# Kernel tuning notes

Measured on AMD Instinct MI355X. Metric: run time of the kernel, lower is better.

Reference implementation:

```python
import jax, jax.numpy as jnp
import numpy as np

HIDDEN = 2048
QUANTILES = 16
BATCH = 8192
HALF = HIDDEN // 2


def setup_inputs() -> dict:
    key = jax.random.key(0)
    kx, k1, kb1, k2 = jax.random.split(key, 4)
    x = jax.random.normal(kx, (BATCH, HIDDEN), dtype=jnp.float32)
    # Stacked per-head params: head q computes Linear(H->H/2) -> GELU -> Linear(H/2->1)
    # PyTorch Linear default init ~ U(-1/sqrt(fan_in), 1/sqrt(fan_in)); last layer kaiming-normal, bias 0.
    lim1 = 1.0 / np.sqrt(HIDDEN)
    W1 = jax.random.uniform(k1, (QUANTILES, HIDDEN, HALF), minval=-lim1, maxval=lim1, dtype=jnp.float32)
    b1 = jax.random.uniform(kb1, (QUANTILES, HALF), minval=-lim1, maxval=lim1, dtype=jnp.float32)
    # kaiming_normal fan_in, linear nonlinearity -> std = 1/sqrt(fan_in)
    W2 = jax.random.normal(k2, (QUANTILES, HALF), dtype=jnp.float32) / np.sqrt(HALF)
    b2 = jnp.zeros((QUANTILES,), dtype=jnp.float32)
    return {"x": x, "W1": W1, "b1": b1, "W2": W2, "b2": b2}


def reference(x, W1, b1, W2, b2):
    # Batched over all quantile heads: one grouped GEMM + fused GELU + grouped GEMV.
    # h: [batch, quantiles, half]
    h = jnp.einsum('bh,qhk->bqk', x, W1) + b1[None, :, :]
    h = jax.nn.gelu(h, approximate=False)  # torch nn.GELU() default = exact erf GELU
    # out: [batch, quantiles]
    out = jnp.einsum('bqk,qk->bq', h, W2) + b2[None, :]
    return out
```

## Files before the change

### kernel.cpp

```cpp
#include <hip/hip_runtime.h>

#define HIDDEN 2048
#define QUANT  16
#define BATCH  8192
#define HALFD  1024

#define BM 256
#define BN 256
#define BKT 32
#define NT (HIDDEN / BKT)
#define A_HALFS (BM * BKT)
#define SLOT_HALFS (2 * A_HALFS)

typedef _Float16 half8  __attribute__((ext_vector_type(8)));
typedef float    floatx16 __attribute__((ext_vector_type(16)));

__device__ __forceinline__ void load_lds16(const void* gptr, void* lptr) {
  __builtin_amdgcn_global_load_lds(
      (const __attribute__((address_space(1))) void*)gptr,
      (__attribute__((address_space(3))) void*)lptr, 16, 0, 0);
}

__device__ __forceinline__ float gelu_exact(float v) {
  const float z  = 0.7071067811865476f * v;
  const float az = fabsf(z);
  const float t  = __builtin_amdgcn_rcpf(1.0f + 0.3275911f * az);
  const float p  = t * (0.254829592f +
                   t * (-0.284496736f +
                   t * (1.421413741f +
                   t * (-1.453152027f +
                   t * 1.061405429f))));
  float er = 1.0f - p * __expf(-az * az);
  er = copysignf(er, z);
  return 0.5f * v * (1.0f + er);
}

__global__ __launch_bounds__(256) void convert_x_kernel(const float* __restrict__ x,
                                                        _Float16* __restrict__ xh) {
  const int i = (blockIdx.x * 256 + threadIdx.x) * 8;
  const float4 a = *(const float4*)(x + i);
  const float4 b = *(const float4*)(x + i + 4);
  half8 h;
  h[0] = (_Float16)a.x; h[1] = (_Float16)a.y; h[2] = (_Float16)a.z; h[3] = (_Float16)a.w;
  h[4] = (_Float16)b.x; h[5] = (_Float16)b.y; h[6] = (_Float16)b.z; h[7] = (_Float16)b.w;
  *(half8*)(xh + i) = h;
}

__global__ __launch_bounds__(256) void transpose_w1_kernel(const float* __restrict__ W1,
                                                           _Float16* __restrict__ W1T) {
  __shared__ float tile[64][33];
  const int q  = blockIdx.z;
  const int h0 = blockIdx.y * 64;
  const int n0 = blockIdx.x * 32;
  const float* src = W1 + (size_t)q * HIDDEN * HALFD;
  _Float16*    dst = W1T + (size_t)q * HALFD * HIDDEN;
  const int t  = threadIdx.x;
  const int lr = t >> 3;
  const int lc = (t & 7) * 4;
  #pragma unroll
  for (int j = 0; j < 2; ++j) {
    const float4 v = *(const float4*)(src + (size_t)(h0 + lr + 32 * j) * HALFD + n0 + lc);
    tile[lr + 32 * j][lc + 0] = v.x;
    tile[lr + 32 * j][lc + 1] = v.y;
    tile[lr + 32 * j][lc + 2] = v.z;
    tile[lr + 32 * j][lc + 3] = v.w;
  }
  __syncthreads();
  const int sn = t >> 3;
  const int sh = (t & 7) * 8;
  half8 v;
  #pragma unroll
  for (int c = 0; c < 8; ++c) v[c] = (_Float16)tile[sh + c][sn];
  *(half8*)(dst + (size_t)(n0 + sn) * HIDDEN + h0 + sh) = v;
}

__global__ __launch_bounds__(256) void init_out_kernel(float* __restrict__ out,
                                                       const float* __restrict__ b2) {
  const int i = blockIdx.x * 256 + threadIdx.x;
  out[i] = b2[i & (QUANT - 1)];
}

__global__ __launch_bounds__(512, 2) void qhead_gemm_kernel(
    const _Float16* __restrict__ A,
    const _Float16* __restrict__ BT,
    const float* __restrict__ b1,
    const float* __restrict__ W2,
    float* __restrict__ out) {
  extern __shared__ _Float16 lds[];

  const int tid  = threadIdx.x;
  const int lane = tid & 63;
  const int wave = tid >> 6;
  const int wm = wave >> 2, wn = wave & 3;
  const int r31 = lane & 31, l5 = lane >> 5;
  const int fsw = (r31 >> 1) & 3;

  const int flat = blockIdx.x;
  const int wg = (flat & 7) * 256 + (flat >> 3);
  const int mb = wg >> 6;
  const int qn = wg & 63;
  const int q  = qn >> 2;
  const int nb = qn & 3;
  const int m0 = mb << 8;

  const _Float16* Ablk = A + (size_t)m0 * HIDDEN;
  const _Float16* Bblk = BT + ((size_t)q * HALFD + nb * BN) * HIDDEN;

  const int srow = tid >> 2;
  const int skg  = (tid & 3) ^ ((srow >> 1) & 3);
  const _Float16* agp = Ablk + (size_t)srow * HIDDEN + skg * 8;
  const _Float16* bgp = Bblk + (size_t)srow * HIDDEN + skg * 8;

  int aoff[4], boff[2];
  #pragma unroll
  for (int mf = 0; mf < 4; ++mf) aoff[mf] = (wm * 128 + mf * 32 + r31) * BKT;
  #pragma unroll
  for (int nf = 0; nf < 2; ++nf) boff[nf] = (wn * 64 + nf * 32 + r31) * BKT + A_HALFS;

  floatx16 acc[4][2];
  #pragma unroll
  for (int mf = 0; mf < 4; ++mf)
    #pragma unroll
    for (int nf = 0; nf < 2; ++nf)
      #pragma unroll
      for (int i = 0; i < 16; ++i) acc[mf][nf][i] = 0.f;

#define STAGE(ts_) do {                                                    \
    const int ts = (ts_);                                                  \
    const int kc = ((ts < NT) ? ts : (ts - NT)) * BKT;   \
    _Float16* ld = lds + (ts & 3) * SLOT_HALFS + tid * 8;                  \
    load_lds16(agp + kc, ld);                                              \
    load_lds16(agp + kc + (size_t)128 * HIDDEN, ld + 4096);                \
    load_lds16(bgp + kc, ld + A_HALFS);                                    \
    load_lds16(bgp + kc + (size_t)128 * HIDDEN, ld + A_HALFS + 4096);      \
  } while (0)

  STAGE(0); STAGE(1); STAGE(2);
  asm volatile("s_waitcnt vmcnt(8)\n\ts_barrier" ::: "memory");

  #pragma unroll 4
  for (int t = 0; t < NT; ++t) {
    STAGE(t + 3);
    const _Float16* ls = lds + (t & 3) * SLOT_HALFS;
    __builtin_amdgcn_s_setprio(1);
    #pragma unroll
    for (int ks = 0; ks < 2; ++ks) {
      const int p = (((ks << 1) | l5) ^ fsw) << 3;
      half8 af[4], bf[2];
      #pragma unroll
      for (int mf = 0; mf < 4; ++mf) af[mf] = *(const half8*)(ls + aoff[mf] + p);
      #pragma unroll
      for (int nf = 0; nf < 2; ++nf) bf[nf] = *(const half8*)(ls + boff[nf] + p);
      #pragma unroll
      for (int mf = 0; mf < 4; ++mf)
        #pragma unroll
        for (int nf = 0; nf < 2; ++nf)
          acc[mf][nf] = __builtin_amdgcn_mfma_f32_32x32x16_f16(af[mf], bf[nf], acc[mf][nf], 0, 0, 0);
    }
    __builtin_amdgcn_s_setprio(0);
    asm volatile("s_waitcnt vmcnt(8) lgkmcnt(0)\n\ts_barrier" ::: "memory");
  }
#undef STAGE

  const int colb = nb * BN + wn * 64;
  #pragma unroll
  for (int mf = 0; mf < 4; ++mf) {
    float rs[16];
    #pragma unroll
    for (int r = 0; r < 16; ++r) rs[r] = 0.f;
    #pragma unroll
    for (int nf = 0; nf < 2; ++nf) {
      const int ncol = colb + nf * 32 + r31;
      const float b1v = b1[q * HALFD + ncol];
      const float w2v = W2[q * HALFD + ncol];
      #pragma unroll
      for (int r = 0; r < 16; ++r)
        rs[r] += gelu_exact(acc[mf][nf][r] + b1v) * w2v;
    }
    #pragma unroll
    for (int r = 0; r < 16; ++r) {
      float v = rs[r];
      v += __shfl_xor(v, 1, 64);
      v += __shfl_xor(v, 2, 64);
      v += __shfl_xor(v, 4, 64);
      v += __shfl_xor(v, 8, 64);
      v += __shfl_xor(v, 16, 64);
      rs[r] = v;
    }
    if (r31 == 0) {
      const int mbase = m0 + wm * 128 + mf * 32 + 4 * l5;
      #pragma unroll
      for (int r = 0; r < 16; ++r) {
        const int mrow = mbase + (r & 3) + 8 * (r >> 2);
        atomicAdd(&out[(size_t)mrow * QUANT + q], rs[r]);
      }
    }
  }
}

extern "C" void kernel_launch(void* const* d_in, const int* in_sizes, int n_in,
                              void* d_out, int out_size, void* d_ws, size_t ws_size,
                              hipStream_t stream) {
  const float* x  = (const float*)d_in[0];
  const float* W1 = (const float*)d_in[1];
  const float* b1 = (const float*)d_in[2];
  const float* W2 = (const float*)d_in[3];
  const float* b2 = (const float*)d_in[4];
  float* out = (float*)d_out;

  _Float16* xh  = (_Float16*)d_ws;
  _Float16* w1t = (_Float16*)((char*)d_ws +
                  (size_t)BATCH * HIDDEN * sizeof(_Float16));

  static int lds_cfg = 0;
  if (!lds_cfg) {
    hipFuncSetAttribute(reinterpret_cast<const void*>(qhead_gemm_kernel),
                        hipFuncAttributeMaxDynamicSharedMemorySize, 131072);
    lds_cfg = 1;
  }

  convert_x_kernel<<<BATCH * HIDDEN / (256 * 8), 256, 0, stream>>>(x, xh);
  transpose_w1_kernel<<<dim3(HALFD / 32, HIDDEN / 64, QUANT), 256, 0, stream>>>(W1, w1t);
  init_out_kernel<<<BATCH * QUANT / 256, 256, 0, stream>>>(out, b2);
  qhead_gemm_kernel<<<dim3(BATCH / BM * (QUANT * HALFD / BN)), 512, 131072, stream>>>(
      xh, w1t, b1, W2, out);
}
```

Measured before the change: 918.2 us.

## Split K-step into barrier-synchronized phases interleaving A/B staging with MFMA

Restructures the main GEMM loop into four phases per pair of K-tiles. Each phase issues its LDS fragment reads and half of a global-to-LDS stage (A or B), then runs its 8 MFMAs between explicit barriers and sched_barriers. The aim is to interleave memory issue with matrix work in a ping-pong style across waves and spread the vmcnt waits. It adds twice as many barriers per tile, and the correctness of the waitcnt accounting with split stages is delicate.

```diff
diff --git a/kernel.cpp b/kernel.cpp
--- a/kernel.cpp
+++ b/kernel.cpp
@@ -9,6 +9,7 @@
 #define BN 256
 #define BKT 32
 #define NT (HIDDEN / BKT)
+#define NT2 (NT / 2)
 #define A_HALFS (BM * BKT)
 #define SLOT_HALFS (2 * A_HALFS)
 
@@ -125,42 +126,65 @@
       #pragma unroll
       for (int i = 0; i < 16; ++i) acc[mf][nf][i] = 0.f;
 
-#define STAGE(ts_) do {                                                    \
-    const int ts = (ts_);                                                  \
-    const int kc = ((ts < NT) ? ts : (ts - NT)) * BKT;   \
-    _Float16* ld = lds + (ts & 3) * SLOT_HALFS + tid * 8;                  \
-    load_lds16(agp + kc, ld);                                              \
-    load_lds16(agp + kc + (size_t)128 * HIDDEN, ld + 4096);                \
-    load_lds16(bgp + kc, ld + A_HALFS);                                    \
-    load_lds16(bgp + kc + (size_t)128 * HIDDEN, ld + A_HALFS + 4096);      \
+#define STAGE_A(ts_) do {                                                  \
+    const int ts_a = (ts_);                                                \
+    const int kc_a = ((ts_a < NT) ? ts_a : (ts_a - NT)) * BKT;             \
+    _Float16* ld_a = lds + (ts_a & 3) * SLOT_HALFS + tid * 8;              \
+    load_lds16(agp + kc_a, ld_a);                                          \
+    load_lds16(agp + kc_a + (size_t)128 * HIDDEN, ld_a + 4096);            \
   } while (0)
 
-  STAGE(0); STAGE(1); STAGE(2);
+#define STAGE_B(ts_) do {                                                  \
+    const int ts_b = (ts_);                                                \
+    const int kc_b = ((ts_b < NT) ? ts_b : (ts_b - NT)) * BKT;             \
+    _Float16* ld_b = lds + (ts_b & 3) * SLOT_HALFS + A_HALFS + tid * 8;    \
+    load_lds16(bgp + kc_b, ld_b);                                          \
+    load_lds16(bgp + kc_b + (size_t)128 * HIDDEN, ld_b + 4096);            \
+  } while (0)
+
+#define PHASE(LS, KS, STAGE_STMT, DO_VM) do {                              \
+    const _Float16* ls_ = (LS);                                            \
+    const int p_ = (((KS << 1) | l5) ^ fsw) << 3;                          \
+    half8 af0 = *(const half8*)(ls_ + aoff[0] + p_);                       \
+    half8 af1 = *(const half8*)(ls_ + aoff[1] + p_);                       \
+    half8 af2 = *(const half8*)(ls_ + aoff[2] + p_);                       \
+    half8 af3 = *(const half8*)(ls_ + aoff[3] + p_);                       \
+    half8 bf0 = *(const half8*)(ls_ + boff[0] + p_);                       \
+    half8 bf1 = *(const half8*)(ls_ + boff[1] + p_);                       \
+    STAGE_STMT;                                                            \
+    asm volatile("s_barrier" ::: "memory");                                \
+    asm volatile("s_waitcnt lgkmcnt(0)" ::: "memory");                     \
+    __builtin_amdgcn_sched_barrier(0);                                     \
+    __builtin_amdgcn_s_setprio(1);                                         \
+    acc[0][0] = __builtin_amdgcn_mfma_f32_32x32x16_f16(af0, bf0, acc[0][0], 0, 0, 0); \
+    acc[0][1] = __builtin_amdgcn_mfma_f32_32x32x16_f16(af0, bf1, acc[0][1], 0, 0, 0); \
+    acc[1][0] = __builtin_amdgcn_mfma_f32_32x32x16_f16(af1, bf0, acc[1][0], 0, 0, 0); \
+    acc[1][1] = __builtin_amdgcn_mfma_f32_32x32x16_f16(af1, bf1, acc[1][1], 0, 0, 0); \
+    acc[2][0] = __builtin_amdgcn_mfma_f32_32x32x16_f16(af2, bf0, acc[2][0], 0, 0, 0); \
+    acc[2][1] = __builtin_amdgcn_mfma_f32_32x32x16_f16(af2, bf1, acc[2][1], 0, 0, 0); \
+    acc[3][0] = __builtin_amdgcn_mfma_f32_32x32x16_f16(af3, bf0, acc[3][0], 0, 0, 0); \
+    acc[3][1] = __builtin_amdgcn_mfma_f32_32x32x16_f16(af3, bf1, acc[3][1], 0, 0, 0); \
+    __builtin_amdgcn_s_setprio(0);                                         \
+    __builtin_amdgcn_sched_barrier(0);                                     \
+    if (DO_VM) asm volatile("s_waitcnt vmcnt(8)" ::: "memory");            \
+    asm volatile("s_barrier" ::: "memory");                                \
+  } while (0)
+
+  STAGE_A(0); STAGE_B(0); STAGE_A(1); STAGE_B(1); STAGE_A(2); STAGE_B(2);
   asm volatile("s_waitcnt vmcnt(8)\n\ts_barrier" ::: "memory");
 
-  #pragma unroll 4
-  for (int t = 0; t < NT; ++t) {
-    STAGE(t + 3);
-    const _Float16* ls = lds + (t & 3) * SLOT_HALFS;
-    __builtin_amdgcn_s_setprio(1);
-    #pragma unroll
-    for (int ks = 0; ks < 2; ++ks) {
-      const int p = (((ks << 1) | l5) ^ fsw) << 3;
-      half8 af[4], bf[2];
-      #pragma unroll
-      for (int mf = 0; mf < 4; ++mf) af[mf] = *(const half8*)(ls + aoff[mf] + p);
-      #pragma unroll
-      for (int nf = 0; nf < 2; ++nf) bf[nf] = *(const half8*)(ls + boff[nf] + p);
-      #pragma unroll
-      for (int mf = 0; mf < 4; ++mf)
-        #pragma unroll
-        for (int nf = 0; nf < 2; ++nf)
-          acc[mf][nf] = __builtin_amdgcn_mfma_f32_32x32x16_f16(af[mf], bf[nf], acc[mf][nf], 0, 0, 0);
-    }
-    __builtin_amdgcn_s_setprio(0);
-    asm volatile("s_waitcnt vmcnt(8) lgkmcnt(0)\n\ts_barrier" ::: "memory");
-  }
-#undef STAGE
+  #pragma unroll 2
+  for (int t = 0; t < NT2; ++t) {
+    const _Float16* ls0 = lds + ((2 * t) & 3) * SLOT_HALFS;
+    const _Float16* ls1 = lds + ((2 * t + 1) & 3) * SLOT_HALFS;
+    PHASE(ls0, 0, STAGE_A(2 * t + 3), 0);
+    PHASE(ls0, 1, STAGE_B(2 * t + 3), 1);
+    PHASE(ls1, 0, STAGE_A(2 * t + 4), 0);
+    PHASE(ls1, 1, STAGE_B(2 * t + 4), 1);
+  }
+#undef PHASE
+#undef STAGE_A
+#undef STAGE_B
 
   const int colb = nb * BN + wn * 64;
   #pragma unroll
```

Result: faster. 881.0 us (-4.1%).
